# Kernel optimization log

Hardware: AMD Instinct MI355X
Metric: run time of the kernel (lower is better)

## Reference

```python
import jax, jax.numpy as jnp
import numpy as np

N_CELLS = 50000
N_GENES = 2000
HIDDEN = 128
HEADS = 4
HEAD_DIM = HIDDEN // HEADS
E_FULL = 800000
E_PRUNED = 400000
LN_EPS = 1e-6
NEG_SLOPE = 0.2


def setup_inputs() -> dict:
    key = jax.random.key(0)
    ks = jax.random.split(key, 20)
    s_in = 1.0 / np.sqrt(N_GENES)
    s_h = 1.0 / np.sqrt(HIDDEN)
    inp = {
        "node_features": jax.random.normal(ks[0], (N_CELLS, N_GENES), jnp.float32),
        "full_edge_index": jax.random.randint(ks[1], (2, E_FULL), 0, N_CELLS, jnp.int64 if jax.config.jax_enable_x64 else jnp.int32),
        "full_edge_weights": jax.random.uniform(ks[2], (E_FULL, 1), jnp.float32),
        "pruned_edge_index": jax.random.randint(ks[3], (2, E_PRUNED), 0, N_CELLS, jnp.int64 if jax.config.jax_enable_x64 else jnp.int32),
        "pruned_edge_weights": jax.random.uniform(ks[4], (E_PRUNED, 1), jnp.float32),
        "alpha": jax.random.uniform(ks[5], (), jnp.float32),
        # input projection
        "ip_w": jax.random.normal(ks[6], (N_GENES, HIDDEN), jnp.float32) * s_in,
        "ip_b": jnp.zeros((HIDDEN,), jnp.float32),
        # GAT full graph
        "gf_wsrc": jax.random.normal(ks[7], (HIDDEN, HIDDEN), jnp.float32) * s_h,
        "gf_wdst": jax.random.normal(ks[8], (HIDDEN, HIDDEN), jnp.float32) * s_h,
        "gf_wedge": jax.random.normal(ks[9], (1, HIDDEN), jnp.float32),
        "gf_attn": jax.random.normal(ks[10], (HEADS, HEAD_DIM), jnp.float32) * (1.0 / np.sqrt(HEAD_DIM)),
        "gf_bias": jnp.zeros((HIDDEN,), jnp.float32),
        # GAT pruned graph
        "gp_wsrc": jax.random.normal(ks[11], (HIDDEN, HIDDEN), jnp.float32) * s_h,
        "gp_wdst": jax.random.normal(ks[12], (HIDDEN, HIDDEN), jnp.float32) * s_h,
        "gp_wedge": jax.random.normal(ks[13], (1, HIDDEN), jnp.float32),
        "gp_attn": jax.random.normal(ks[14], (HEADS, HEAD_DIM), jnp.float32) * (1.0 / np.sqrt(HEAD_DIM)),
        "gp_bias": jnp.zeros((HIDDEN,), jnp.float32),
        # LayerNorm
        "ln_scale": jnp.ones((HIDDEN,), jnp.float32),
        "ln_bias": jnp.zeros((HIDDEN,), jnp.float32),
    }
    return inp


def _gatv2(h, edge_index, edge_w, wsrc, wdst, wedge, attn, bias):
    """GATv2 with edge features: e_ij = a_h . leaky_relu(Ws h_i + Wd h_j + We w_ij),
    segment-softmax over destination nodes, scatter-aggregate Ws h_src, concat heads."""
    n = h.shape[0]
    src, dst = edge_index[0], edge_index[1]
    hs = (h @ wsrc).reshape(n, HEADS, HEAD_DIM)
    hd = (h @ wdst).reshape(n, HEADS, HEAD_DIM)
    ew = (edge_w @ wedge).reshape(-1, HEADS, HEAD_DIM)  # [E,H,D]
    z = jax.nn.leaky_relu(hs[src] + hd[dst] + ew, NEG_SLOPE)  # [E,H,D]
    logits = jnp.einsum('ehd,hd->eh', z, attn)  # [E,H]
    # segment softmax over incoming edges of each dst node
    m = jax.ops.segment_max(logits, dst, num_segments=n)
    m = jnp.where(jnp.isfinite(m), m, 0.0)
    ex = jnp.exp(logits - m[dst])
    denom = jax.ops.segment_sum(ex, dst, num_segments=n)
    att = ex / (denom[dst] + 1e-16)  # [E,H]
    out = jax.ops.segment_sum(att[..., None] * hs[src], dst, num_segments=n)  # [n,H,D]
    return out.reshape(n, HIDDEN) + bias


def _layer_norm(x, scale, bias):
    mu = jnp.mean(x, axis=-1, keepdims=True)
    var = jnp.mean(jnp.square(x - mu), axis=-1, keepdims=True)
    return (x - mu) * jax.lax.rsqrt(var + LN_EPS) * scale + bias


def reference(node_features, full_edge_index, full_edge_weights, pruned_edge_index,
              pruned_edge_weights, alpha, ip_w, ip_b,
              gf_wsrc, gf_wdst, gf_wedge, gf_attn, gf_bias,
              gp_wsrc, gp_wdst, gp_wedge, gp_attn, gp_bias,
              ln_scale, ln_bias):
    h = node_features @ ip_w + ip_b  # [n, hidden]
    h_full = _gatv2(h, full_edge_index, full_edge_weights, gf_wsrc, gf_wdst, gf_wedge, gf_attn, gf_bias)
    h_pruned = _gatv2(h, pruned_edge_index, pruned_edge_weights, gp_wsrc, gp_wdst, gp_wedge, gp_attn, gp_bias)
    h = (1.0 - alpha) * h_full + alpha * h_pruned
    h = jax.nn.elu(h)
    return _layer_norm(h, ln_scale, ln_bias)
```

## Files before the change

### kernel.cpp

```cpp
#include <hip/hip_runtime.h>
#include <hip/hip_bf16.h>

#define N_GENES 2000
#define SA 72

typedef __attribute__((ext_vector_type(8))) short frag8;
typedef __attribute__((ext_vector_type(4))) float facc4;

static __device__ __forceinline__ unsigned short f2bf(float f) {
    unsigned int u = __float_as_uint(f);
    unsigned int r = (u + 0x7FFFu + ((u >> 16) & 1u)) >> 16;
    return (unsigned short)r;
}
static __device__ __forceinline__ float bf2f(unsigned short s) {
    return __uint_as_float(((unsigned int)s) << 16);
}
static __device__ __forceinline__ ushort2 pk2(float a, float b) {
    __hip_bfloat162 r = __float22bfloat162_rn(float2{a, b});
    return *(ushort2*)&r;
}

__global__ void prep(const float* __restrict__ ip_w,
                     const float* __restrict__ ws_f, const float* __restrict__ wd_f,
                     const float* __restrict__ ws_p, const float* __restrict__ wd_p,
                     unsigned short* __restrict__ Bt1,
                     unsigned short* __restrict__ Bf, unsigned short* __restrict__ Bp) {
    int idx = blockIdx.x * blockDim.x + threadIdx.x;
    if (idx < 128 * 2048) {
        int nrow = idx >> 11, k = idx & 2047;
        unsigned short v = 0;
        if (k < N_GENES) v = f2bf(ip_w[(size_t)k * 128 + nrow]);
        Bt1[idx] = v;
    } else {
        int q = idx - 128 * 2048;
        if (q >= 2 * 256 * 128) return;
        int g = q >> 15;
        int r = (q >> 7) & 255;
        int k = q & 127;
        const float* w = (g == 0) ? (r < 128 ? ws_f : wd_f) : (r < 128 ? ws_p : wd_p);
        (g == 0 ? Bf : Bp)[(r << 7) | k] = f2bf(w[k * 128 + (r & 127)]);
    }
}

__global__ __launch_bounds__(256) void gemm1(const float* __restrict__ A,
                                             const unsigned short* __restrict__ Bt,
                                             const float* __restrict__ bias,
                                             unsigned short* __restrict__ Cb, int M, int K) {
    const int Kpad = 2048;
    __shared__ __align__(16) unsigned short lA[64 * SA];
    int t = threadIdx.x, lane = t & 63, wv = t >> 6;
    int lr = lane & 15, lq = lane >> 4;
    facc4 acc[4][2];
#pragma unroll
    for (int i = 0; i < 4; i++)
#pragma unroll
        for (int j = 0; j < 2; j++) acc[i][j] = (facc4){0.f, 0.f, 0.f, 0.f};
    int row_base = blockIdx.x * 64;

    int ar_r[4], ar_c[4];
    const float* ar_p[4];
#pragma unroll
    for (int j = 0; j < 4; j++) {
        int q = j * 256 + t;
        ar_r[j] = q >> 4;
        ar_c[j] = (q & 15) * 4;
        int rg = row_base + ar_r[j];
        if (rg >= M) rg = M - 1;
        ar_p[j] = A + (size_t)rg * K + ar_c[j];
    }
    const unsigned short* bp[4];
#pragma unroll
    for (int ks = 0; ks < 2; ks++)
#pragma unroll
        for (int ni = 0; ni < 2; ni++) {
            int col = wv * 32 + ni * 16 + lr;
            bp[ks * 2 + ni] = Bt + (size_t)col * Kpad + ks * 32 + lq * 8;
        }

    float4 ar[4];
    frag8 bfr[4];
#pragma unroll
    for (int j = 0; j < 4; j++) ar[j] = *(const float4*)(ar_p[j]);
#pragma unroll
    for (int f = 0; f < 4; f++) bfr[f] = *(const frag8*)(bp[f]);

    for (int k0 = 0; k0 < Kpad; k0 += 64) {
        __syncthreads();
#pragma unroll
        for (int j = 0; j < 4; j++) {
            ushort2 u01 = pk2(ar[j].x, ar[j].y);
            ushort2 u23 = pk2(ar[j].z, ar[j].w);
            ushort4 u = {u01.x, u01.y, u23.x, u23.y};
            *(ushort4*)&lA[ar_r[j] * SA + ar_c[j]] = u;
        }
        __syncthreads();
        int kn = k0 + 64;
        frag8 bfn[4];
        if (kn < Kpad) {
#pragma unroll
            for (int j = 0; j < 4; j++) {
                int kk = kn + ar_c[j];
                float4 v = {0.f, 0.f, 0.f, 0.f};
                if (kk < K) v = *(const float4*)(ar_p[j] + kn);
                ar[j] = v;
            }
#pragma unroll
            for (int f = 0; f < 4; f++) bfn[f] = *(const frag8*)(bp[f] + kn);
        }
#pragma unroll
        for (int ks = 0; ks < 2; ks++) {
            frag8 af[4];
#pragma unroll
            for (int mi = 0; mi < 4; mi++)
                af[mi] = *(const frag8*)&lA[(mi * 16 + lr) * SA + ks * 32 + lq * 8];
#pragma unroll
            for (int mi = 0; mi < 4; mi++)
#pragma unroll
                for (int ni = 0; ni < 2; ni++)
                    acc[mi][ni] = __builtin_amdgcn_mfma_f32_16x16x32_bf16(af[mi], bfr[ks * 2 + ni], acc[mi][ni], 0, 0, 0);
        }
        if (kn < Kpad) {
#pragma unroll
            for (int f = 0; f < 4; f++) bfr[f] = bfn[f];
        }
    }
#pragma unroll
    for (int mi = 0; mi < 4; mi++) {
#pragma unroll
        for (int r = 0; r < 4; r++) {
            int row = row_base + mi * 16 + lq * 4 + r;
            if (row < M) {
#pragma unroll
                for (int ni = 0; ni < 2; ni++) {
                    int col = wv * 32 + ni * 16 + lr;
                    Cb[(size_t)row * 128 + col] = f2bf(acc[mi][ni][r] + bias[col]);
                }
            }
        }
    }
}

__global__ __launch_bounds__(256) void gemm_hshd(const unsigned short* __restrict__ A,
                                                 const unsigned short* __restrict__ Bf,
                                                 const unsigned short* __restrict__ Bp,
                                                 unsigned short* __restrict__ Cf,
                                                 unsigned short* __restrict__ Cp, int M) {
    const int K = 128, NT = 256, CF = 4;
    const unsigned short* Bt = blockIdx.y ? Bp : Bf;
    unsigned short* Cb = blockIdx.y ? Cp : Cf;
    __shared__ __align__(16) unsigned short lA[64 * SA];
    __shared__ __align__(16) unsigned short lB[NT * SA];
    int t = threadIdx.x, lane = t & 63, wv = t >> 6;
    int lr = lane & 15, lq = lane >> 4;
    facc4 acc[4][CF];
#pragma unroll
    for (int i = 0; i < 4; i++)
#pragma unroll
        for (int j = 0; j < CF; j++) acc[i][j] = (facc4){0.f, 0.f, 0.f, 0.f};
    int row_base = blockIdx.x * 64;

    for (int k0 = 0; k0 < K; k0 += 64) {
        __syncthreads();
#pragma unroll
        for (int j = 0; j < 2; j++) {
            int q = j * 256 + t;
            int r = q >> 3, off = (q & 7) * 8;
            int rg = row_base + r; if (rg >= M) rg = M - 1;
            *(uint4*)&lA[r * SA + off] = *(const uint4*)(A + (size_t)rg * K + k0 + off);
        }
#pragma unroll
        for (int j = 0; j < 8; j++) {
            int q = j * 256 + t;
            int r = q >> 3, off = (q & 7) * 8;
            *(uint4*)&lB[r * SA + off] = *(const uint4*)(Bt + (size_t)r * K + k0 + off);
        }
        __syncthreads();
#pragma unroll
        for (int ks = 0; ks < 2; ks++) {
            frag8 af[4], bf[CF];
#pragma unroll
            for (int mi = 0; mi < 4; mi++)
                af[mi] = *(const frag8*)&lA[(mi * 16 + lr) * SA + ks * 32 + lq * 8];
#pragma unroll
            for (int ni = 0; ni < CF; ni++)
                bf[ni] = *(const frag8*)&lB[(wv * 16 * CF + ni * 16 + lr) * SA + ks * 32 + lq * 8];
#pragma unroll
            for (int mi = 0; mi < 4; mi++)
#pragma unroll
                for (int ni = 0; ni < CF; ni++)
                    acc[mi][ni] = __builtin_amdgcn_mfma_f32_16x16x32_bf16(af[mi], bf[ni], acc[mi][ni], 0, 0, 0);
        }
    }
#pragma unroll
    for (int mi = 0; mi < 4; mi++) {
#pragma unroll
        for (int r = 0; r < 4; r++) {
            int row = row_base + mi * 16 + lq * 4 + r;
            if (row < M) {
#pragma unroll
                for (int ni = 0; ni < CF; ni++) {
                    int col = wv * 16 * CF + ni * 16 + lr;
                    Cb[(size_t)row * NT + col] = f2bf(acc[mi][ni][r]);
                }
            }
        }
    }
}

__global__ void deg2(const int* __restrict__ dst_f, int Ef,
                     const int* __restrict__ dst_p, int Ep,
                     int* __restrict__ deg, int N) {
    int e = blockIdx.x * blockDim.x + threadIdx.x;
    if (e < Ef) atomicAdd(&deg[dst_f[e]], 1);
    else if (e < Ef + Ep) atomicAdd(&deg[N + dst_p[e - Ef]], 1);
}

__global__ __launch_bounds__(256) void scan_part(const int* __restrict__ in,
                                                 int* __restrict__ bsum, int n) {
    int t = threadIdx.x, b = blockIdx.x;
    int lane = t & 63, wv = t >> 6;
    int base = b * 2048 + t * 8;
    int s = 0;
    if (base + 7 < n) {
        int4 v0 = *(const int4*)(in + base);
        int4 v1 = *(const int4*)(in + base + 4);
        s = v0.x + v0.y + v0.z + v0.w + v1.x + v1.y + v1.z + v1.w;
    } else {
#pragma unroll
        for (int j = 0; j < 8; j++) if (base + j < n) s += in[base + j];
    }
#pragma unroll
    for (int o = 32; o >= 1; o >>= 1) s += __shfl_xor(s, o);
    __shared__ int red[4];
    if (lane == 0) red[wv] = s;
    __syncthreads();
    if (t == 0) bsum[b] = red[0] + red[1] + red[2] + red[3];
}

__global__ __launch_bounds__(256) void scan_tops(int* __restrict__ bsum, int nb,
                                                 int* __restrict__ offs, int n) {
    __shared__ int buf[256];
    int t = threadIdx.x;
    int orig = (t < nb) ? bsum[t] : 0;
    int v = orig;
    buf[t] = v;
    __syncthreads();
    for (int o = 1; o < 256; o <<= 1) {
        int y = (t >= o) ? buf[t - o] : 0;
        __syncthreads();
        v += y;
        buf[t] = v;
        __syncthreads();
    }
    if (t < nb) bsum[t] = v - orig;
    if (t == nb - 1) offs[n] = v;
}

__global__ __launch_bounds__(256) void scan_final(const int* __restrict__ in,
                                                  const int* __restrict__ bsum,
                                                  int* __restrict__ offs, int n) {
    int t = threadIdx.x, b = blockIdx.x;
    int lane = t & 63, wv = t >> 6;
    int base = b * 2048 + t * 8;
    int a[8];
#pragma unroll
    for (int j = 0; j < 8; j++) a[j] = (base + j < n) ? in[base + j] : 0;
    int s = a[0] + a[1] + a[2] + a[3] + a[4] + a[5] + a[6] + a[7];
    int incl = s;
#pragma unroll
    for (int o = 1; o < 64; o <<= 1) {
        int y = __shfl_up(incl, o);
        if (lane >= o) incl += y;
    }
    __shared__ int wsum[4];
    if (lane == 63) wsum[wv] = incl;
    __syncthreads();
    int wpre = 0;
#pragma unroll
    for (int j = 0; j < 4; j++) if (j < wv) wpre += wsum[j];
    int excl = incl - s + wpre + bsum[b];
#pragma unroll
    for (int j = 0; j < 8; j++) {
        if (base + j < n) offs[base + j] = excl;
        excl += a[j];
    }
}

__global__ void fill2(const int* __restrict__ src_f, const int* __restrict__ dst_f,
                      const float* __restrict__ ew_f, int Ef,
                      const int* __restrict__ src_p, const int* __restrict__ dst_p,
                      const float* __restrict__ ew_p, int Ep,
                      const int* __restrict__ offs, int* __restrict__ deg,
                      int2* __restrict__ srcw, int N) {
    int e = blockIdx.x * blockDim.x + threadIdx.x;
    if (e >= Ef + Ep) return;
    int g = (e >= Ef);
    int ee = g ? e - Ef : e;
    int d = g ? dst_p[ee] : dst_f[ee];
    int node = g ? N + d : d;
    int p = offs[node] + atomicAdd(&deg[node], -1) - 1;
    int s = g ? src_p[ee] : src_f[ee];
    float w = g ? ew_p[ee] : ew_f[ee];
    srcw[p] = make_int2(s, __float_as_int(w));
}

__global__ __launch_bounds__(256) void gat2(const int* __restrict__ offs,
                                            const int2* __restrict__ srcw,
                                            const unsigned short* __restrict__ hshd_f,
                                            const unsigned short* __restrict__ hshd_p,
                                            const float* __restrict__ wedge_f,
                                            const float* __restrict__ attn_f,
                                            const float* __restrict__ bias_f,
                                            const float* __restrict__ wedge_p,
                                            const float* __restrict__ attn_p,
                                            const float* __restrict__ bias_p,
                                            float* __restrict__ out_full,
                                            float* __restrict__ out_pruned, int N) {
    int node = blockIdx.x * 4 + (threadIdx.x >> 6);
    if (node >= 2 * N) return;
    int g = node >= N;
    int onode = g ? node - N : node;
    const unsigned short* hshd = g ? hshd_p : hshd_f;
    const float* wedge = g ? wedge_p : wedge_f;
    const float* attn = g ? attn_p : attn_f;
    const float* bias = g ? bias_p : bias_f;
    float* out = g ? out_pruned : out_full;
    int lane = threadIdx.x & 63;
    int d2 = lane * 2;
    const float2 wv = *(const float2*)&wedge[d2];
    const float2 av = *(const float2*)&attn[d2];
    unsigned int hdraw = *(const unsigned int*)&hshd[(size_t)onode * 256 + 128 + d2];
    const float hd0 = __uint_as_float(hdraw << 16);
    const float hd1 = __uint_as_float(hdraw & 0xffff0000u);
    int s = offs[node], cnt = offs[node + 1] - s;
    float m = -INFINITY, l = 0.f, acc0 = 0.f, acc1 = 0.f;
    if (cnt > 0) {
        int last = s + cnt - 1;
        auto CL = [last](int j) { return j > last ? last : j; };
        int2 e0 = srcw[s], e1 = srcw[CL(s + 1)], e2 = srcw[CL(s + 2)], e3 = srcw[CL(s + 3)];
        int2 e4 = srcw[CL(s + 4)], e5 = srcw[CL(s + 5)];
        unsigned int hr0 = *(const unsigned int*)&hshd[(size_t)e0.x * 256 + d2];
        unsigned int hr1 = *(const unsigned int*)&hshd[(size_t)e1.x * 256 + d2];
        unsigned int hr2 = *(const unsigned int*)&hshd[(size_t)e2.x * 256 + d2];
        unsigned int hr3 = *(const unsigned int*)&hshd[(size_t)e3.x * 256 + d2];
        for (int i = 0; i < cnt; i += 2) {
            int2 e6 = srcw[CL(s + i + 6)], e7 = srcw[CL(s + i + 7)];
            unsigned int hr4 = *(const unsigned int*)&hshd[(size_t)e4.x * 256 + d2];
            unsigned int hr5 = *(const unsigned int*)&hshd[(size_t)e5.x * 256 + d2];
            {
                float h0 = __uint_as_float(hr0 << 16);
                float h1 = __uint_as_float(hr0 & 0xffff0000u);
                float w = __int_as_float(e0.y);
                float z0 = fmaf(w, wv.x, h0 + hd0); z0 = (z0 > 0.f) ? z0 : 0.2f * z0;
                float z1 = fmaf(w, wv.y, h1 + hd1); z1 = (z1 > 0.f) ? z1 : 0.2f * z1;
                float t = z0 * av.x + z1 * av.y;
                t += __shfl_xor(t, 1);
                t += __shfl_xor(t, 2);
                t += __shfl_xor(t, 4);
                t += __shfl_xor(t, 8);
                float mn = fmaxf(m, t);
                float sc = __expf(m - mn), p = __expf(t - mn);
                l = l * sc + p;
                acc0 = acc0 * sc + p * h0;
                acc1 = acc1 * sc + p * h1;
                m = mn;
            }
            if (i + 1 < cnt) {
                float h0 = __uint_as_float(hr1 << 16);
                float h1 = __uint_as_float(hr1 & 0xffff0000u);
                float w = __int_as_float(e1.y);
                float z0 = fmaf(w, wv.x, h0 + hd0); z0 = (z0 > 0.f) ? z0 : 0.2f * z0;
                float z1 = fmaf(w, wv.y, h1 + hd1); z1 = (z1 > 0.f) ? z1 : 0.2f * z1;
                float t = z0 * av.x + z1 * av.y;
                t += __shfl_xor(t, 1);
                t += __shfl_xor(t, 2);
                t += __shfl_xor(t, 4);
                t += __shfl_xor(t, 8);
                float mn = fmaxf(m, t);
                float sc = __expf(m - mn), p = __expf(t - mn);
                l = l * sc + p;
                acc0 = acc0 * sc + p * h0;
                acc1 = acc1 * sc + p * h1;
                m = mn;
            }
            e0 = e2; e1 = e3; e2 = e4; e3 = e5; e4 = e6; e5 = e7;
            hr0 = hr2; hr1 = hr3; hr2 = hr4; hr3 = hr5;
        }
    }
    float inv = 1.f / (l + 1e-16f);
    const float2 bv = *(const float2*)&bias[d2];
    float2 o;
    o.x = acc0 * inv + bv.x;
    o.y = acc1 * inv + bv.y;
    *(float2*)&out[(size_t)onode * 128 + d2] = o;
}

__global__ __launch_bounds__(256) void final_kernel(const float* __restrict__ hf,
                                                    float* __restrict__ out,
                                                    const float* __restrict__ alpha_p,
                                                    const float* __restrict__ scale,
                                                    const float* __restrict__ beta, int n) {
    int node = blockIdx.x * 4 + (threadIdx.x >> 6);
    if (node >= n) return;
    int lane = threadIdx.x & 63;
    int d2 = lane * 2;
    float a = *alpha_p;
    float2 f = *(const float2*)&hf[(size_t)node * 128 + d2];
    float2 p = *(const float2*)&out[(size_t)node * 128 + d2];
    float x0 = (1.f - a) * f.x + a * p.x;
    float x1 = (1.f - a) * f.y + a * p.y;
    x0 = (x0 > 0.f) ? x0 : expm1f(x0);
    x1 = (x1 > 0.f) ? x1 : expm1f(x1);
    float sm = x0 + x1;
#pragma unroll
    for (int o = 32; o >= 1; o >>= 1) sm += __shfl_xor(sm, o);
    float mu = sm * (1.f / 128.f);
    float d0 = x0 - mu, d1 = x1 - mu;
    float v = d0 * d0 + d1 * d1;
#pragma unroll
    for (int o = 32; o >= 1; o >>= 1) v += __shfl_xor(v, o);
    float rstd = rsqrtf(v * (1.f / 128.f) + 1e-6f);
    const float2 sv = *(const float2*)&scale[d2];
    const float2 bv = *(const float2*)&beta[d2];
    float2 o2;
    o2.x = d0 * rstd * sv.x + bv.x;
    o2.y = d1 * rstd * sv.y + bv.y;
    *(float2*)&out[(size_t)node * 128 + d2] = o2;
}

extern "C" void kernel_launch(void* const* d_in, const int* in_sizes, int n_in,
                              void* d_out, int out_size, void* d_ws, size_t ws_size,
                              hipStream_t stream) {
    const float* nf = (const float*)d_in[0];
    const int* fei = (const int*)d_in[1];
    const float* few = (const float*)d_in[2];
    const int* pei = (const int*)d_in[3];
    const float* pew = (const float*)d_in[4];
    const float* alpha = (const float*)d_in[5];
    const float* ip_w = (const float*)d_in[6];
    const float* ip_b = (const float*)d_in[7];
    const float* gf_wsrc = (const float*)d_in[8];
    const float* gf_wdst = (const float*)d_in[9];
    const float* gf_wedge = (const float*)d_in[10];
    const float* gf_attn = (const float*)d_in[11];
    const float* gf_bias = (const float*)d_in[12];
    const float* gp_wsrc = (const float*)d_in[13];
    const float* gp_wdst = (const float*)d_in[14];
    const float* gp_wedge = (const float*)d_in[15];
    const float* gp_attn = (const float*)d_in[16];
    const float* gp_bias = (const float*)d_in[17];
    const float* ln_scale = (const float*)d_in[18];
    const float* ln_bias = (const float*)d_in[19];

    const int N = in_sizes[0] / N_GENES;
    const int Ef = in_sizes[1] / 2;
    const int Ep = in_sizes[3] / 2;
    const int Etot = Ef + Ep;
    const int n2 = 2 * N;

    char* base = (char*)d_ws;
    size_t off = 0;
    auto carve = [&](size_t bytes) -> char* {
        char* p = base + off;
        off = (off + bytes + 255) & ~(size_t)255;
        return p;
    };
    unsigned short* Bt1 = (unsigned short*)carve((size_t)128 * 2048 * 2);
    unsigned short* Bf = (unsigned short*)carve(256 * 128 * 2);
    unsigned short* Bp = (unsigned short*)carve(256 * 128 * 2);
    unsigned short* h_bf = (unsigned short*)carve((size_t)N * 128 * 2);
    unsigned short* hshd_f = (unsigned short*)carve((size_t)N * 256 * 2);
    unsigned short* hshd_p = (unsigned short*)carve((size_t)N * 256 * 2);
    float* h_full = (float*)carve((size_t)N * 128 * 4);
    int* deg = (int*)carve((size_t)n2 * 4);
    int* offs = (int*)carve((size_t)(n2 + 4) * 4);
    int* bsum = (int*)carve(256 * 4);
    int2* srcw = (int2*)carve((size_t)Etot * 8);
    float* out_f = (float*)d_out;

    prep<<<(128 * 2048 + 2 * 256 * 128 + 255) / 256, 256, 0, stream>>>(
        ip_w, gf_wsrc, gf_wdst, gp_wsrc, gp_wdst, Bt1, Bf, Bp);

    int gb1 = (N + 63) / 64;
    gemm1<<<gb1, 256, 0, stream>>>(nf, Bt1, ip_b, h_bf, N, N_GENES);
    gemm_hshd<<<dim3(gb1, 2), 256, 0, stream>>>(h_bf, Bf, Bp, hshd_f, hshd_p, N);

    const int* src_f = fei;
    const int* dst_f = fei + Ef;
    const int* src_p = pei;
    const int* dst_p = pei + Ep;
    hipMemsetAsync(deg, 0, (size_t)n2 * 4, stream);
    deg2<<<(Etot + 255) / 256, 256, 0, stream>>>(dst_f, Ef, dst_p, Ep, deg, N);
    int nb = (n2 + 2047) / 2048;
    scan_part<<<nb, 256, 0, stream>>>(deg, bsum, n2);
    scan_tops<<<1, 256, 0, stream>>>(bsum, nb, offs, n2);
    scan_final<<<nb, 256, 0, stream>>>(deg, bsum, offs, n2);
    fill2<<<(Etot + 255) / 256, 256, 0, stream>>>(src_f, dst_f, few, Ef, src_p, dst_p, pew, Ep,
                                                  offs, deg, srcw, N);

    gat2<<<(n2 + 3) / 4, 256, 0, stream>>>(offs, srcw, hshd_f, hshd_p,
                                           gf_wedge, gf_attn, gf_bias,
                                           gp_wedge, gp_attn, gp_bias,
                                           h_full, out_f, N);

    final_kernel<<<(N + 3) / 4, 256, 0, stream>>>(h_full, out_f, alpha, ln_scale, ln_bias, N);
    (void)ws_size; (void)n_in; (void)out_size;
}
```

Measured before the change: 865.8 us.

## Fuse input projection with src/dst projection GEMM, deepen gather prefetch, use exp2

Merges the input projection GEMM and the per-graph source/destination projection GEMM into one kernel. The bf16 hidden tile is staged in shared memory and multiplied by both weight sets, so the h intermediate is never written to or read from global memory. The degree memset is folded into the prep kernel, and the GAT gather loop prefetches edges and source rows two steps further ahead. exp is replaced with exp2, with log2(e) pre-scaled into the attention vector. The risks are higher register and LDS pressure in the fused kernel and B fragments read directly from global memory.

```diff
diff --git a/kernel.cpp b/kernel.cpp
--- a/kernel.cpp
+++ b/kernel.cpp
@@ -3,6 +3,7 @@
 
 #define N_GENES 2000
 #define SA 72
+#define SH 136
 
 typedef __attribute__((ext_vector_type(8))) short frag8;
 typedef __attribute__((ext_vector_type(4))) float facc4;
@@ -24,8 +25,10 @@
                      const float* __restrict__ ws_f, const float* __restrict__ wd_f,
                      const float* __restrict__ ws_p, const float* __restrict__ wd_p,
                      unsigned short* __restrict__ Bt1,
-                     unsigned short* __restrict__ Bf, unsigned short* __restrict__ Bp) {
+                     unsigned short* __restrict__ Bf, unsigned short* __restrict__ Bp,
+                     int* __restrict__ deg, int n2) {
     int idx = blockIdx.x * blockDim.x + threadIdx.x;
+    if (idx < n2) deg[idx] = 0;
     if (idx < 128 * 2048) {
         int nrow = idx >> 11, k = idx & 2047;
         unsigned short v = 0;
@@ -42,12 +45,17 @@
     }
 }
 
-__global__ __launch_bounds__(256) void gemm1(const float* __restrict__ A,
-                                             const unsigned short* __restrict__ Bt,
-                                             const float* __restrict__ bias,
-                                             unsigned short* __restrict__ Cb, int M, int K) {
+__global__ __launch_bounds__(256) void gemm_fused(const float* __restrict__ A,
+                                                  const unsigned short* __restrict__ Bt,
+                                                  const float* __restrict__ bias,
+                                                  const unsigned short* __restrict__ Bf,
+                                                  const unsigned short* __restrict__ Bp,
+                                                  unsigned short* __restrict__ Cf,
+                                                  unsigned short* __restrict__ Cp,
+                                                  int M, int K) {
     const int Kpad = 2048;
     __shared__ __align__(16) unsigned short lA[64 * SA];
+    __shared__ __align__(16) unsigned short lH[64 * SH];
     int t = threadIdx.x, lane = t & 63, wv = t >> 6;
     int lr = lane & 15, lq = lane >> 4;
     facc4 acc[4][2];
@@ -124,83 +132,55 @@
             for (int f = 0; f < 4; f++) bfr[f] = bfn[f];
         }
     }
+    __syncthreads();
 #pragma unroll
     for (int mi = 0; mi < 4; mi++) {
 #pragma unroll
         for (int r = 0; r < 4; r++) {
-            int row = row_base + mi * 16 + lq * 4 + r;
-            if (row < M) {
-#pragma unroll
-                for (int ni = 0; ni < 2; ni++) {
-                    int col = wv * 32 + ni * 16 + lr;
-                    Cb[(size_t)row * 128 + col] = f2bf(acc[mi][ni][r] + bias[col]);
-                }
+            int row = mi * 16 + lq * 4 + r;
+#pragma unroll
+            for (int ni = 0; ni < 2; ni++) {
+                int col = wv * 32 + ni * 16 + lr;
+                lH[row * SH + col] = f2bf(acc[mi][ni][r] + bias[col]);
             }
         }
     }
-}
-
-__global__ __launch_bounds__(256) void gemm_hshd(const unsigned short* __restrict__ A,
-                                                 const unsigned short* __restrict__ Bf,
-                                                 const unsigned short* __restrict__ Bp,
-                                                 unsigned short* __restrict__ Cf,
-                                                 unsigned short* __restrict__ Cp, int M) {
-    const int K = 128, NT = 256, CF = 4;
-    const unsigned short* Bt = blockIdx.y ? Bp : Bf;
-    unsigned short* Cb = blockIdx.y ? Cp : Cf;
-    __shared__ __align__(16) unsigned short lA[64 * SA];
-    __shared__ __align__(16) unsigned short lB[NT * SA];
-    int t = threadIdx.x, lane = t & 63, wv = t >> 6;
-    int lr = lane & 15, lq = lane >> 4;
-    facc4 acc[4][CF];
-#pragma unroll
-    for (int i = 0; i < 4; i++)
-#pragma unroll
-        for (int j = 0; j < CF; j++) acc[i][j] = (facc4){0.f, 0.f, 0.f, 0.f};
-    int row_base = blockIdx.x * 64;
-
-    for (int k0 = 0; k0 < K; k0 += 64) {
-        __syncthreads();
-#pragma unroll
-        for (int j = 0; j < 2; j++) {
-            int q = j * 256 + t;
-            int r = q >> 3, off = (q & 7) * 8;
-            int rg = row_base + r; if (rg >= M) rg = M - 1;
-            *(uint4*)&lA[r * SA + off] = *(const uint4*)(A + (size_t)rg * K + k0 + off);
-        }
-#pragma unroll
-        for (int j = 0; j < 8; j++) {
-            int q = j * 256 + t;
-            int r = q >> 3, off = (q & 7) * 8;
-            *(uint4*)&lB[r * SA + off] = *(const uint4*)(Bt + (size_t)r * K + k0 + off);
-        }
-        __syncthreads();
-#pragma unroll
-        for (int ks = 0; ks < 2; ks++) {
-            frag8 af[4], bf[CF];
+    __syncthreads();
+#pragma unroll 1
+    for (int g = 0; g < 2; g++) {
+        const unsigned short* B2 = g ? Bp : Bf;
+        unsigned short* Cb = g ? Cp : Cf;
+        facc4 a2[4][4];
+#pragma unroll
+        for (int i = 0; i < 4; i++)
+#pragma unroll
+            for (int j = 0; j < 4; j++) a2[i][j] = (facc4){0.f, 0.f, 0.f, 0.f};
+#pragma unroll
+        for (int ks = 0; ks < 4; ks++) {
+            frag8 af[4], bf[4];
 #pragma unroll
             for (int mi = 0; mi < 4; mi++)
-                af[mi] = *(const frag8*)&lA[(mi * 16 + lr) * SA + ks * 32 + lq * 8];
-#pragma unroll
-            for (int ni = 0; ni < CF; ni++)
-                bf[ni] = *(const frag8*)&lB[(wv * 16 * CF + ni * 16 + lr) * SA + ks * 32 + lq * 8];
+                af[mi] = *(const frag8*)&lH[(mi * 16 + lr) * SH + ks * 32 + lq * 8];
+#pragma unroll
+            for (int ni = 0; ni < 4; ni++)
+                bf[ni] = *(const frag8*)(B2 + ((wv * 64 + ni * 16 + lr) << 7) + ks * 32 + lq * 8);
 #pragma unroll
             for (int mi = 0; mi < 4; mi++)
 #pragma unroll
-                for (int ni = 0; ni < CF; ni++)
-                    acc[mi][ni] = __builtin_amdgcn_mfma_f32_16x16x32_bf16(af[mi], bf[ni], acc[mi][ni], 0, 0, 0);
-        }
-    }
-#pragma unroll
-    for (int mi = 0; mi < 4; mi++) {
-#pragma unroll
-        for (int r = 0; r < 4; r++) {
-            int row = row_base + mi * 16 + lq * 4 + r;
-            if (row < M) {
-#pragma unroll
-                for (int ni = 0; ni < CF; ni++) {
-                    int col = wv * 16 * CF + ni * 16 + lr;
-                    Cb[(size_t)row * NT + col] = f2bf(acc[mi][ni][r]);
+                for (int ni = 0; ni < 4; ni++)
+                    a2[mi][ni] = __builtin_amdgcn_mfma_f32_16x16x32_bf16(af[mi], bf[ni], a2[mi][ni], 0, 0, 0);
+        }
+#pragma unroll
+        for (int mi = 0; mi < 4; mi++) {
+#pragma unroll
+            for (int r = 0; r < 4; r++) {
+                int row = row_base + mi * 16 + lq * 4 + r;
+                if (row < M) {
+#pragma unroll
+                    for (int ni = 0; ni < 4; ni++) {
+                        int col = wv * 64 + ni * 16 + lr;
+                        Cb[(size_t)row * 256 + col] = f2bf(a2[mi][ni][r]);
+                    }
                 }
             }
         }
@@ -327,8 +307,10 @@
     float* out = g ? out_pruned : out_full;
     int lane = threadIdx.x & 63;
     int d2 = lane * 2;
+    const float LOG2E = 1.4426950408889634f;
     const float2 wv = *(const float2*)&wedge[d2];
-    const float2 av = *(const float2*)&attn[d2];
+    float2 av = *(const float2*)&attn[d2];
+    av.x *= LOG2E; av.y *= LOG2E;
     unsigned int hdraw = *(const unsigned int*)&hshd[(size_t)onode * 256 + 128 + d2];
     const float hd0 = __uint_as_float(hdraw << 16);
     const float hd1 = __uint_as_float(hdraw & 0xffff0000u);
@@ -338,15 +320,18 @@
         int last = s + cnt - 1;
         auto CL = [last](int j) { return j > last ? last : j; };
         int2 e0 = srcw[s], e1 = srcw[CL(s + 1)], e2 = srcw[CL(s + 2)], e3 = srcw[CL(s + 3)];
-        int2 e4 = srcw[CL(s + 4)], e5 = srcw[CL(s + 5)];
+        int2 e4 = srcw[CL(s + 4)], e5 = srcw[CL(s + 5)], e6 = srcw[CL(s + 6)], e7 = srcw[CL(s + 7)];
+        int2 e8 = srcw[CL(s + 8)], e9 = srcw[CL(s + 9)];
         unsigned int hr0 = *(const unsigned int*)&hshd[(size_t)e0.x * 256 + d2];
         unsigned int hr1 = *(const unsigned int*)&hshd[(size_t)e1.x * 256 + d2];
         unsigned int hr2 = *(const unsigned int*)&hshd[(size_t)e2.x * 256 + d2];
         unsigned int hr3 = *(const unsigned int*)&hshd[(size_t)e3.x * 256 + d2];
+        unsigned int hr4 = *(const unsigned int*)&hshd[(size_t)e4.x * 256 + d2];
+        unsigned int hr5 = *(const unsigned int*)&hshd[(size_t)e5.x * 256 + d2];
         for (int i = 0; i < cnt; i += 2) {
-            int2 e6 = srcw[CL(s + i + 6)], e7 = srcw[CL(s + i + 7)];
-            unsigned int hr4 = *(const unsigned int*)&hshd[(size_t)e4.x * 256 + d2];
-            unsigned int hr5 = *(const unsigned int*)&hshd[(size_t)e5.x * 256 + d2];
+            int2 ea = srcw[CL(s + i + 10)], eb = srcw[CL(s + i + 11)];
+            unsigned int hr6 = *(const unsigned int*)&hshd[(size_t)e6.x * 256 + d2];
+            unsigned int hr7 = *(const unsigned int*)&hshd[(size_t)e7.x * 256 + d2];
             {
                 float h0 = __uint_as_float(hr0 << 16);
                 float h1 = __uint_as_float(hr0 & 0xffff0000u);
@@ -359,7 +344,8 @@
                 t += __shfl_xor(t, 4);
                 t += __shfl_xor(t, 8);
                 float mn = fmaxf(m, t);
-                float sc = __expf(m - mn), p = __expf(t - mn);
+                float sc = __builtin_amdgcn_exp2f(m - mn);
+                float p = __builtin_amdgcn_exp2f(t - mn);
                 l = l * sc + p;
                 acc0 = acc0 * sc + p * h0;
                 acc1 = acc1 * sc + p * h1;
@@ -377,14 +363,15 @@
                 t += __shfl_xor(t, 4);
                 t += __shfl_xor(t, 8);
                 float mn = fmaxf(m, t);
-                float sc = __expf(m - mn), p = __expf(t - mn);
+                float sc = __builtin_amdgcn_exp2f(m - mn);
+                float p = __builtin_amdgcn_exp2f(t - mn);
                 l = l * sc + p;
                 acc0 = acc0 * sc + p * h0;
                 acc1 = acc1 * sc + p * h1;
                 m = mn;
             }
-            e0 = e2; e1 = e3; e2 = e4; e3 = e5; e4 = e6; e5 = e7;
-            hr0 = hr2; hr1 = hr3; hr2 = hr4; hr3 = hr5;
+            e0 = e2; e1 = e3; e2 = e4; e3 = e5; e4 = e6; e5 = e7; e6 = e8; e7 = e9; e8 = ea; e9 = eb;
+            hr0 = hr2; hr1 = hr3; hr2 = hr4; hr3 = hr5; hr4 = hr6; hr5 = hr7;
         }
     }
     float inv = 1.f / (l + 1e-16f);
@@ -468,7 +455,6 @@
     unsigned short* Bt1 = (unsigned short*)carve((size_t)128 * 2048 * 2);
     unsigned short* Bf = (unsigned short*)carve(256 * 128 * 2);
     unsigned short* Bp = (unsigned short*)carve(256 * 128 * 2);
-    unsigned short* h_bf = (unsigned short*)carve((size_t)N * 128 * 2);
     unsigned short* hshd_f = (unsigned short*)carve((size_t)N * 256 * 2);
     unsigned short* hshd_p = (unsigned short*)carve((size_t)N * 256 * 2);
     float* h_full = (float*)carve((size_t)N * 128 * 4);
@@ -479,17 +465,15 @@
     float* out_f = (float*)d_out;
 
     prep<<<(128 * 2048 + 2 * 256 * 128 + 255) / 256, 256, 0, stream>>>(
-        ip_w, gf_wsrc, gf_wdst, gp_wsrc, gp_wdst, Bt1, Bf, Bp);
+        ip_w, gf_wsrc, gf_wdst, gp_wsrc, gp_wdst, Bt1, Bf, Bp, deg, n2);
 
     int gb1 = (N + 63) / 64;
-    gemm1<<<gb1, 256, 0, stream>>>(nf, Bt1, ip_b, h_bf, N, N_GENES);
-    gemm_hshd<<<dim3(gb1, 2), 256, 0, stream>>>(h_bf, Bf, Bp, hshd_f, hshd_p, N);
+    gemm_fused<<<gb1, 256, 0, stream>>>(nf, Bt1, ip_b, Bf, Bp, hshd_f, hshd_p, N, N_GENES);
 
     const int* src_f = fei;
     const int* dst_f = fei + Ef;
     const int* src_p = pei;
     const int* dst_p = pei + Ep;
-    hipMemsetAsync(deg, 0, (size_t)n2 * 4, stream);
     deg2<<<(Etot + 255) / 256, 256, 0, stream>>>(dst_f, Ef, dst_p, Ep, deg, N);
     int nb = (n2 + 2047) / 2048;
     scan_part<<<nb, 256, 0, stream>>>(deg, bsum, n2);
```

After: 855.6 us. Within noise of the previous version (-1.2%).
